# Performance work log

Hardware: AMD Instinct MI355X
Metric: run time of the kernel (lower is better)

The kernel has to match this reference:

```python
import math
import jax, jax.numpy as jnp
from jax import lax
import numpy as np

B, M, L = 256, 21, 512
P, S, D = 16, 8, 256
NL, EXP, H, LAM = 3, 2, 96, 0.01
T = (L - P) // S + 1  # 63 patches
HID = D * EXP


def _pos_enc():
    pe = np.zeros((T, D), np.float32)
    pos = np.arange(T, dtype=np.float32)[:, None]
    div = np.exp(np.arange(0, D, 2, dtype=np.float32) * (-math.log(10000.0) / D))
    pe[:, 0::2] = np.sin(pos * div)
    pe[:, 1::2] = np.cos(pos * div)
    return jnp.asarray(pe)


def _clin(zr, zi, Wr, Wi, br, bi):
    # faithful to torch: bias br added to both terms of yr (cancels), bi added twice in yi
    yr = (zr @ Wr.T + br) - (zi @ Wi.T + br)
    yi = (zr @ Wi.T + bi) + (zi @ Wr.T + bi)
    return yr, yi


def _softshrink(zr, zi):
    mag = jnp.sqrt(zr * zr + zi * zi)
    scale = jnp.maximum(mag - LAM, 0.0) / (mag + 1e-8) * (mag > LAM).astype(zr.dtype)
    return zr * scale, zi * scale


def _layernorm(x, g, b):
    mu = jnp.mean(x, -1, keepdims=True)
    var = jnp.mean((x - mu) ** 2, -1, keepdims=True)
    return (x - mu) / jnp.sqrt(var + 1e-5) * g + b


def _block(x, p):
    (Tw, Tb, Gew, Geb, Gpw, Gpb,
     H1Wr, H1Wi, H1br, H1bi, H2Wr, H2Wi, H2br, H2bi, lng, lnb) = p
    g = jax.nn.gelu(x @ Gew.T + Geb, approximate=False) @ Gpw.T + Gpb
    zf = jnp.fft.rfft(x, axis=1)  # FFT along time/patch axis T
    zr, zi = zf.real, zf.imag
    zr, zi = _clin(zr, zi, H1Wr, H1Wi, H1br, H1bi)
    zr, zi = _softshrink(zr, zi)
    zr, zi = _clin(zr, zi, H2Wr, H2Wi, H2br, H2bi)
    pt = jnp.fft.irfft(lax.complex(zr, zi), n=x.shape[1], axis=1)
    out = (g * pt) @ Tw.T + Tb
    return _layernorm(out + x, lng, lnb)


def _forward(x, conv_w, conv_b, tp, sp, gate_w, gate_b, proj_w, proj_b):
    # per-instance, per-variable norm over time (biased std, eps on std)
    mean = jnp.mean(x, -1, keepdims=True)
    std = jnp.sqrt(jnp.mean((x - mean) ** 2, -1, keepdims=True))
    xn = (x - mean) / (std + 1e-5)
    patches = lax.conv_general_dilated(xn, conv_w, (S,), 'VALID',
                                       dimension_numbers=('NCH', 'OIH', 'NCH'))
    patches = patches + conv_b[None, :, None]
    h = patches.transpose(0, 2, 1) + _pos_enc()[None]  # (B, T, D)
    t = h
    s = h
    for i in range(NL):
        t = _block(t, tuple(a[i] for a in tp))
        s = _block(s, tuple(a[i] for a in sp))
    gate = jax.nn.sigmoid(t @ gate_w.T + gate_b)
    feat = gate * t + (1.0 - gate) * s
    out = feat.reshape(feat.shape[0], -1) @ proj_w.T + proj_b
    y = out.reshape(-1, M, H) * (std + 1e-5) + mean
    return y


def setup_inputs() -> dict:
    key = jax.random.key(0)
    ks = iter(jax.random.split(key, 64))

    def nrm(shape, scale):
        return jax.random.normal(next(ks), shape, jnp.float32) * scale

    inp = {'x': nrm((B, M, L), 1.0)}
    inp['conv_w'] = nrm((D, M, P), 1.0 / math.sqrt(M * P))
    inp['conv_b'] = jnp.zeros((D,), jnp.float32)

    def layer_params(prefix):
        d = {}
        d[prefix + 'Tw'] = nrm((NL, D, D), 1.0 / math.sqrt(D))
        d[prefix + 'Tb'] = jnp.zeros((NL, D), jnp.float32)
        d[prefix + 'Gew'] = nrm((NL, HID, D), 1.0 / math.sqrt(D))
        d[prefix + 'Geb'] = jnp.zeros((NL, HID), jnp.float32)
        d[prefix + 'Gpw'] = nrm((NL, D, HID), 1.0 / math.sqrt(HID))
        d[prefix + 'Gpb'] = jnp.zeros((NL, D), jnp.float32)
        for hname in ('H1', 'H2'):
            d[prefix + hname + 'Wr'] = nrm((NL, D, D), 1.0 / math.sqrt(D))
            d[prefix + hname + 'Wi'] = nrm((NL, D, D), 1.0 / math.sqrt(D))
            d[prefix + hname + 'br'] = jnp.zeros((NL, D), jnp.float32)
            d[prefix + hname + 'bi'] = jnp.zeros((NL, D), jnp.float32)
        d[prefix + 'lng'] = jnp.ones((NL, D), jnp.float32)
        d[prefix + 'lnb'] = jnp.zeros((NL, D), jnp.float32)
        return d

    inp.update(layer_params('t_'))
    inp.update(layer_params('s_'))
    inp['gate_w'] = nrm((1, D), 1.0 / math.sqrt(D))
    inp['gate_b'] = jnp.zeros((1,), jnp.float32)
    inp['proj_w'] = nrm((M * H, T * D), 1.0 / math.sqrt(T * D))
    inp['proj_b'] = jnp.zeros((M * H,), jnp.float32)
    return inp


def reference(x, conv_w, conv_b,
              t_Tw, t_Tb, t_Gew, t_Geb, t_Gpw, t_Gpb,
              t_H1Wr, t_H1Wi, t_H1br, t_H1bi, t_H2Wr, t_H2Wi, t_H2br, t_H2bi, t_lng, t_lnb,
              s_Tw, s_Tb, s_Gew, s_Geb, s_Gpw, s_Gpb,
              s_H1Wr, s_H1Wi, s_H1br, s_H1bi, s_H2Wr, s_H2Wi, s_H2br, s_H2bi, s_lng, s_lnb,
              gate_w, gate_b, proj_w, proj_b):
    tp = (t_Tw, t_Tb, t_Gew, t_Geb, t_Gpw, t_Gpb,
          t_H1Wr, t_H1Wi, t_H1br, t_H1bi, t_H2Wr, t_H2Wi, t_H2br, t_H2bi, t_lng, t_lnb)
    sp = (s_Tw, s_Tb, s_Gew, s_Geb, s_Gpw, s_Gpb,
          s_H1Wr, s_H1Wi, s_H1br, s_H1bi, s_H2Wr, s_H2Wi, s_H2br, s_H2bi, s_lng, s_lnb)
    return _forward(x, conv_w, conv_b, tp, sp, gate_w, gate_b, proj_w, proj_b)
```

## Files before the change

kernel.cpp:

```cpp
#include <hip/hip_runtime.h>
#include <cstddef>
#include <cstdint>

#define B_    256
#define M_    21
#define L_    512
#define D_    256
#define T_    63
#define F_    32
#define NT_   16128
#define HID_  512
#define KCP_  352
#define H_    96
#define LAM_  0.01f
#define PZ_   16

typedef __attribute__((ext_vector_type(8))) short short8;
typedef __attribute__((ext_vector_type(4))) float f32x4;
typedef unsigned int u32;
typedef const u32 __attribute__((address_space(1)))* gas1_t;
typedef u32 __attribute__((address_space(3)))* las3_t;

__device__ __forceinline__ void async_copy16(const void* g, void* l) {
  __builtin_amdgcn_global_load_lds((gas1_t)g, (las3_t)(uintptr_t)l, 16, 0, 0);
}
__device__ __forceinline__ unsigned short f2bf(float x) {
  unsigned u = __float_as_uint(x);
  return (unsigned short)((u + 0x7FFF + ((u >> 16) & 1)) >> 16);
}
__device__ __forceinline__ float bf2f(unsigned short u) {
  return __uint_as_float(((unsigned)u) << 16);
}
__device__ __forceinline__ float gelu_exact(float v) {
  return 0.5f * v * (1.0f + erff(v * 0.70710678118654752f));
}
__device__ __forceinline__ float block_sum256(float v, float* red4) {
  #pragma unroll
  for (int off = 32; off > 0; off >>= 1) v += __shfl_down(v, off, 64);
  if ((threadIdx.x & 63) == 0) red4[threadIdx.x >> 6] = v;
  __syncthreads();
  float r = red4[0] + red4[1] + red4[2] + red4[3];
  __syncthreads();
  return r;
}
__device__ __forceinline__ float wave_sum(float v) {
  #pragma unroll
  for (int off = 1; off < 64; off <<= 1) v += __shfl_xor(v, off, 64);
  return v;
}

struct CvtEnt { const float* src; unsigned short* dst; int rows, scol, dcol, blk0; };
struct CvtArgs { CvtEnt e[19]; int nent; };
__global__ __launch_bounds__(256) void wprep_kernel(CvtArgs a) {
  int blk = blockIdx.x, e = 0;
  while (e + 1 < a.nent && a.e[e + 1].blk0 <= blk) ++e;
  CvtEnt en = a.e[e];
  int idx = (blk - en.blk0) * 256 + threadIdx.x;
  int total = en.rows * en.dcol;
  if (idx >= total) return;
  int r = idx / en.dcol, c = idx - r * en.dcol;
  float v = (c < en.scol) ? en.src[(size_t)r * en.scol + c] : 0.f;
  en.dst[idx] = f2bf(v);
}

struct CatArgs { const float* wr[12]; const float* wi[12]; };
__global__ __launch_bounds__(256) void wcat_kernel(CatArgs a, unsigned short* dst) {
  int e = blockIdx.x >> 10;
  int idx = ((blockIdx.x & 1023) << 8) + threadIdx.x;
  int r = idx >> 9, c = idx & 511;
  int cp = r >> 1, p = r & 1, d = c >> 1, q = c & 1;
  const float* wr = a.wr[e];
  const float* wi = a.wi[e];
  float v;
  if (p == 0) v = (q == 0) ? wr[cp * 256 + d] : -wi[cp * 256 + d];
  else        v = (q == 0) ? wi[cp * 256 + d] :  wr[cp * 256 + d];
  dst[(size_t)e * 262144 + idx] = f2bf(v);
}

template <int ACT, int OUTBF, int BIASM, int KSTEPS, int CVTA, int CVTW,
          int SHRINK, int MULPT, int SPLITK, int BK, int RT, int PEW>
__global__ __launch_bounds__(256) void mm_kernel(
    const void* __restrict__ Av,
    const unsigned short* __restrict__ W0, const unsigned short* __restrict__ W1,
    const float* __restrict__ Wf,
    const float* __restrict__ b0, const float* __restrict__ b1,
    const unsigned short* __restrict__ ptb,
    void* __restrict__ Cv,
    const int K, const int Dout, const int ksteps_rt, const int yhalf,
    const int prow, const int totk) {
  constexpr int NP = BK / 32;
  constexpr int RWS = 32 * RT;
  __shared__ __align__(16) unsigned short As[NP * RWS * 32];
  __shared__ __align__(16) unsigned short Bs[NP * 128 * 32];
  const int tid = threadIdx.x, w = tid >> 6, lane = tid & 63;
  const int quad = lane >> 4, r16 = lane & 15;
  int nks = KSTEPS ? KSTEPS : ksteps_rt;
  const int ksbeg = SPLITK ? (int)blockIdx.z * nks : 0;
  if (SPLITK) { int rem = totk - ksbeg; if (nks > rem) nks = rem; }
  const int kst = ksbeg * BK;
  const int tower = ((int)blockIdx.y >= yhalf) ? 1 : 0;
  const unsigned short* Wb = tower ? W1 : W0;
  const float* bias = tower ? b1 : b0;

  const unsigned short* Ab = (const unsigned short*)Av;
  const float* Af = (const float*)Av;
  const unsigned short* gA = nullptr;
  unsigned short* lA = As + (w * 8 * RT) * 32;
  if (!CVTA) gA = Ab + (size_t)((int)blockIdx.y * RWS + w * 8 * RT + (lane >> 2)) * K
                     + kst + (lane & 3) * 8;
  const unsigned short* gB = nullptr;
  unsigned short* lB = Bs + (w * 32) * 32;
  if (!CVTW) gB = Wb + (size_t)((int)blockIdx.x * 128 + w * 32 + (lane >> 2)) * K
                     + kst + (lane & 3) * 8;
  const int crow = tid >> 3;
  const int ck4  = (tid & 7) << 2;

  float4 areg[NP][RT];
  float4 wreg[NP][4];
  auto loadA = [&](int ksi) {
    #pragma unroll
    for (int p = 0; p < NP; ++p)
      #pragma unroll
      for (int rr = 0; rr < RT; ++rr)
        areg[p][rr] = *reinterpret_cast<const float4*>(
            Af + (size_t)((int)blockIdx.y * RWS + crow + 32 * rr) * K
               + kst + ksi * BK + p * 32 + ck4);
  };
  auto loadW = [&](int ksi) {
    #pragma unroll
    for (int p = 0; p < NP; ++p)
      #pragma unroll
      for (int rr = 0; rr < 4; ++rr) {
        int wrow = (int)blockIdx.x * 128 + crow + 32 * rr;
        if (wrow >= Dout) wrow = Dout - 1;
        wreg[p][rr] = *reinterpret_cast<const float4*>(
            Wf + (size_t)wrow * K + kst + ksi * BK + p * 32 + ck4);
      }
  };
  if (CVTA) loadA(0);
  if (CVTW) loadW(0);

  f32x4 acc[RT][4];
  #pragma unroll
  for (int i = 0; i < RT; ++i)
    #pragma unroll
    for (int j = 0; j < 4; ++j)
      #pragma unroll
      for (int r = 0; r < 4; ++r) acc[i][j][r] = 0.f;

  for (int ks = 0; ks < nks; ++ks) {
    if (!CVTA) {
      #pragma unroll
      for (int p = 0; p < NP; ++p)
        #pragma unroll
        for (int c = 0; c < RT / 2; ++c)
          async_copy16(gA + (size_t)(c * 16) * K + p * 32,
                       lA + p * (RWS * 32) + c * 16 * 32);
      gA += BK;
    } else {
      #pragma unroll
      for (int p = 0; p < NP; ++p)
        #pragma unroll
        for (int rr = 0; rr < RT; ++rr) {
          float4 v = areg[p][rr];
          ushort4 o; o.x = f2bf(v.x); o.y = f2bf(v.y); o.z = f2bf(v.z); o.w = f2bf(v.w);
          *reinterpret_cast<ushort4*>(As + p * (RWS * 32) + (crow + 32 * rr) * 32 + ck4) = o;
        }
    }
    if (!CVTW) {
      #pragma unroll
      for (int p = 0; p < NP; ++p) {
        async_copy16(gB + p * 32, lB + p * 4096);
        async_copy16(gB + (size_t)16 * K + p * 32, lB + p * 4096 + 16 * 32);
      }
      gB += BK;
    } else {
      #pragma unroll
      for (int p = 0; p < NP; ++p)
        #pragma unroll
        for (int rr = 0; rr < 4; ++rr) {
          float4 v = wreg[p][rr];
          ushort4 o; o.x = f2bf(v.x); o.y = f2bf(v.y); o.z = f2bf(v.z); o.w = f2bf(v.w);
          *reinterpret_cast<ushort4*>(Bs + p * 4096 + (crow + 32 * rr) * 32 + ck4) = o;
        }
    }
    __syncthreads();
    if (CVTA && ks + 1 < nks) loadA(ks + 1);
    if (CVTW && ks + 1 < nks) loadW(ks + 1);
    #pragma unroll
    for (int p = 0; p < NP; ++p) {
      const unsigned short* pa = As + p * (RWS * 32) + ((w >> 1) * 16 * RT + r16) * 32 + quad * 8;
      const unsigned short* pb = Bs + p * 4096 + (64 * (w & 1) + r16) * 32 + quad * 8;
      short8 af[RT], bfv[4];
      #pragma unroll
      for (int i = 0; i < RT; ++i) af[i] = *reinterpret_cast<const short8*>(pa + i * 512);
      #pragma unroll
      for (int j = 0; j < 4; ++j) bfv[j] = *reinterpret_cast<const short8*>(pb + j * 512);
      #pragma unroll
      for (int i = 0; i < RT; ++i)
        #pragma unroll
        for (int j = 0; j < 4; ++j)
          acc[i][j] = __builtin_amdgcn_mfma_f32_16x16x32_bf16(af[i], bfv[j], acc[i][j], 0, 0, 0);
    }
    __syncthreads();
  }

  float* Cf = (float*)Cv;
  unsigned short* Cb = (unsigned short*)Cv;
  if (SPLITK) Cf += (size_t)blockIdx.z * prow * Dout;
  const int colb = (int)blockIdx.x * 128 + 64 * (w & 1) + r16;
  const int rowb = (int)blockIdx.y * RWS + 16 * RT * (w >> 1) + quad * 4;
  #pragma unroll
  for (int j = 0; j < 4; ++j) {
    int col = colb + 16 * j;
    float bv = 0.f;
    if (BIASM == 0) bv = bias[col];
    else if (BIASM == 1) bv = (col & 1) ? 2.0f * bias[col >> 1] : 0.f;
    bool colok = (BIASM != 2) || (col < Dout);
    #pragma unroll
    for (int i = 0; i < RT; ++i) {
      #pragma unroll
      for (int r = 0; r < 4; ++r) {
        int row = rowb + 16 * i + r;
        float v = acc[i][j][r] + bv;
        if (ACT == 1) v = gelu_exact(v);
        if (SHRINK) {
          float o = __shfl_xor(v, 1, 64);
          float mag = sqrtf(v * v + o * o);
          float s = (mag > LAM_) ? (mag - LAM_) / (mag + 1e-8f) : 0.f;
          v *= s;
        }
        if (MULPT) v *= bf2f(ptb[(size_t)row * Dout + col]);
        if (colok) {
          if (PEW) {
            int t = row % T_;
            float freq = expf((float)(col & ~1) * (-9.210340371976184f / 256.0f));
            float ang = (float)t * freq;
            float pe = (col & 1) ? cosf(ang) : sinf(ang);
            float h = v + pe;
            Cf[(size_t)row * Dout + col] = h;
            Cf[(size_t)row * Dout + col + (size_t)NT_ * D_] = h;
          } else if (OUTBF) {
            Cb[(size_t)row * Dout + col] = f2bf(v);
          } else {
            Cf[(size_t)row * Dout + col] = v;
          }
        }
      }
    }
  }
}

__global__ __launch_bounds__(256) void twln_kernel(
    const unsigned short* __restrict__ A,
    const unsigned short* __restrict__ W0, const unsigned short* __restrict__ W1,
    const float* __restrict__ b0, const float* __restrict__ b1,
    const float* __restrict__ lg0, const float* __restrict__ lb0,
    const float* __restrict__ lg1, const float* __restrict__ lb1,
    float* __restrict__ x32) {
  __shared__ __align__(16) unsigned short As[2][64 * 32];
  __shared__ __align__(16) unsigned short Bs[2][256 * 32];
  const int tid = threadIdx.x, w = tid >> 6, lane = tid & 63;
  const int quad = lane >> 4, r16 = lane & 15;
  const int rh = w >> 1, ch = w & 1;
  const int by = blockIdx.x;
  const int tower = (by >= 252) ? 1 : 0;
  const unsigned short* W = tower ? W1 : W0;
  const float* bias = tower ? b1 : b0;
  const float* lng = tower ? lg1 : lg0;
  const float* lnb = tower ? lb1 : lb0;

  const unsigned short* gA = A + (size_t)(by * 64 + (tid >> 2)) * 256 + (tid & 3) * 8;
  const unsigned short* gW = W + (size_t)(tid >> 2) * 256 + (tid & 3) * 8;

  f32x4 acc[2][8];
  #pragma unroll
  for (int i = 0; i < 2; ++i)
    #pragma unroll
    for (int j = 0; j < 8; ++j)
      #pragma unroll
      for (int r = 0; r < 4; ++r) acc[i][j][r] = 0.f;

  for (int ks = 0; ks < 4; ++ks) {
    #pragma unroll
    for (int p = 0; p < 2; ++p)
      async_copy16(gA + p * 32, (char*)As + p * 4096 + tid * 16);
    #pragma unroll
    for (int p = 0; p < 2; ++p)
      #pragma unroll
      for (int k = 0; k < 4; ++k)
        async_copy16(gW + (size_t)k * 16384 + p * 32,
                     (char*)Bs + p * 16384 + k * 4096 + tid * 16);
    gA += 64; gW += 64;
    __syncthreads();
    #pragma unroll
    for (int p = 0; p < 2; ++p) {
      const unsigned short* pa = As[p] + (rh * 32 + r16) * 32 + quad * 8;
      const unsigned short* pb = Bs[p] + (ch * 128 + r16) * 32 + quad * 8;
      short8 af[2], bfv[8];
      #pragma unroll
      for (int i = 0; i < 2; ++i) af[i] = *reinterpret_cast<const short8*>(pa + i * 512);
      #pragma unroll
      for (int j = 0; j < 8; ++j) bfv[j] = *reinterpret_cast<const short8*>(pb + j * 512);
      #pragma unroll
      for (int i = 0; i < 2; ++i)
        #pragma unroll
        for (int j = 0; j < 8; ++j)
          acc[i][j] = __builtin_amdgcn_mfma_f32_16x16x32_bf16(af[i], bfv[j], acc[i][j], 0, 0, 0);
    }
    __syncthreads();
  }

  const int rowb = by * 64 + rh * 32 + quad * 4;
  const int colb = ch * 128 + r16;
  float s[2][4], sq[2][4];
  #pragma unroll
  for (int i = 0; i < 2; ++i)
    #pragma unroll
    for (int r = 0; r < 4; ++r) { s[i][r] = 0.f; sq[i][r] = 0.f; }
  #pragma unroll
  for (int j = 0; j < 8; ++j) {
    int col = colb + j * 16;
    float bv = bias[col];
    #pragma unroll
    for (int i = 0; i < 2; ++i)
      #pragma unroll
      for (int r = 0; r < 4; ++r) {
        int row = rowb + i * 16 + r;
        float h = acc[i][j][r] + bv + x32[(size_t)row * 256 + col];
        acc[i][j][r] = h;
        s[i][r] += h;
        sq[i][r] += h * h;
      }
  }
  #pragma unroll
  for (int off = 1; off < 16; off <<= 1)
    #pragma unroll
    for (int i = 0; i < 2; ++i)
      #pragma unroll
      for (int r = 0; r < 4; ++r) {
        s[i][r]  += __shfl_xor(s[i][r],  off, 64);
        sq[i][r] += __shfl_xor(sq[i][r], off, 64);
      }
  float* red = (float*)As;
  if (r16 == 0) {
    #pragma unroll
    for (int i = 0; i < 2; ++i)
      #pragma unroll
      for (int r = 0; r < 4; ++r) {
        int lr = rh * 32 + i * 16 + quad * 4 + r;
        red[lr * 4 + ch * 2]     = s[i][r];
        red[lr * 4 + ch * 2 + 1] = sq[i][r];
      }
  }
  __syncthreads();
  #pragma unroll
  for (int i = 0; i < 2; ++i)
    #pragma unroll
    for (int r = 0; r < 4; ++r) {
      int lr = rh * 32 + i * 16 + quad * 4 + r;
      float tot = red[lr * 4] + red[lr * 4 + 2];
      float tsq = red[lr * 4 + 1] + red[lr * 4 + 3];
      float mu = tot * (1.0f / 256.0f);
      float var = tsq * (1.0f / 256.0f) - mu * mu;
      float is = rsqrtf(var + 1e-5f);
      int row = rowb + i * 16 + r;
      #pragma unroll
      for (int j = 0; j < 8; ++j) {
        int col = colb + j * 16;
        x32[(size_t)row * 256 + col] = (acc[i][j][r] - mu) * is * lng[col] + lnb[col];
      }
    }
}

__global__ __launch_bounds__(256) void norm_kernel(const float* __restrict__ x,
    float* __restrict__ xn, float* __restrict__ meanb, float* __restrict__ stdb) {
  __shared__ float red[4];
  int bm = blockIdx.x;
  const float* xr = x + (size_t)bm * L_;
  float v0 = xr[threadIdx.x], v1 = xr[threadIdx.x + 256];
  float mu = block_sum256(v0 + v1, red) * (1.0f / L_);
  float d0 = v0 - mu, d1 = v1 - mu;
  float sd = sqrtf(block_sum256(d0 * d0 + d1 * d1, red) * (1.0f / L_));
  float inv = 1.0f / (sd + 1e-5f);
  float* xo = xn + (size_t)bm * L_;
  xo[threadIdx.x] = d0 * inv;
  xo[threadIdx.x + 256] = d1 * inv;
  if (threadIdx.x == 0) { meanb[bm] = mu; stdb[bm] = sd; }
}

__global__ __launch_bounds__(256) void im2col_kernel(const float* __restrict__ xn,
                                                     unsigned short* __restrict__ im) {
  int row = blockIdx.x;
  int b = row / T_, t = row - b * T_;
  const float* xb = xn + (size_t)b * M_ * L_ + t * 8;
  unsigned short* o = im + (size_t)row * KCP_;
  for (int i = threadIdx.x; i < KCP_; i += 256) {
    float v = 0.f;
    if (i < 336) { int m = i >> 4, p = i & 15; v = xb[m * L_ + p]; }
    o[i] = f2bf(v);
  }
}

__global__ __launch_bounds__(256) void dft_kernel(const float* __restrict__ X,
                                                  unsigned short* __restrict__ Zcat) {
  __shared__ float2 tw[T_ * F_];
  int bt = blockIdx.x, d = threadIdx.x;
  for (int i = threadIdx.x; i < T_ * F_; i += 256) {
    int t = i >> 5, f = i & 31;
    int k = (f * t) % T_;
    float sn, cs;
    sincosf((6.283185307179586f / 63.0f) * (float)k, &sn, &cs);
    tw[i] = make_float2(cs, -sn);
  }
  __syncthreads();
  const float* xb = X + (size_t)bt * T_ * D_ + d;
  float ar[F_], ai[F_];
  #pragma unroll
  for (int f = 0; f < F_; ++f) { ar[f] = 0.f; ai[f] = 0.f; }
  for (int t = 0; t < T_; ++t) {
    float v = xb[(size_t)t * D_];
    const float2* w = &tw[t * F_];
    #pragma unroll
    for (int f = 0; f < F_; ++f) {
      float2 c = w[f];
      ar[f] = fmaf(v, c.x, ar[f]);
      ai[f] = fmaf(v, c.y, ai[f]);
    }
  }
  u32* z = reinterpret_cast<u32*>(Zcat + (size_t)bt * F_ * 512);
  #pragma unroll
  for (int f = 0; f < F_; ++f)
    z[f * 256 + d] = (u32)f2bf(ar[f]) | ((u32)f2bf(ai[f]) << 16);
}

__global__ __launch_bounds__(256) void irfft_kernel(const unsigned short* __restrict__ Y,
                                                    unsigned short* __restrict__ ptb) {
  __shared__ float2 tw[T_ * 31];
  int bt = blockIdx.x, d = threadIdx.x;
  for (int i = threadIdx.x; i < T_ * 31; i += 256) {
    int t = i / 31, f = i - t * 31 + 1;
    int k = (f * t) % T_;
    float sn, cs;
    sincosf((6.283185307179586f / 63.0f) * (float)k, &sn, &cs);
    tw[i] = make_float2(cs * (2.0f / 63.0f), -sn * (2.0f / 63.0f));
  }
  __syncthreads();
  const unsigned short* yb = Y + (size_t)bt * F_ * 512 + 2 * d;
  float y0 = bf2f(yb[0]) * (1.0f / 63.0f);
  float yr[31], yi[31];
  #pragma unroll
  for (int f = 1; f < F_; ++f) {
    u32 p = *reinterpret_cast<const u32*>(yb + (size_t)f * 512);
    yr[f - 1] = bf2f((unsigned short)(p & 0xffff));
    yi[f - 1] = bf2f((unsigned short)(p >> 16));
  }
  unsigned short* po = ptb + (size_t)bt * T_ * D_ + d;
  for (int t = 0; t < T_; ++t) {
    const float2* w = &tw[t * 31];
    float acc0 = y0, acc1 = 0.f;
    #pragma unroll
    for (int f = 0; f < 31; f += 2) {
      float2 c = w[f];
      acc0 = fmaf(yr[f], c.x, fmaf(yi[f], c.y, acc0));
      if (f + 1 < 31) {
        float2 c1 = w[f + 1];
        acc1 = fmaf(yr[f + 1], c1.x, fmaf(yi[f + 1], c1.y, acc1));
      }
    }
    po[(size_t)t * D_] = f2bf(acc0 + acc1);
  }
}

__global__ __launch_bounds__(256) void gate_feat_kernel(const float* __restrict__ x32,
    const float* __restrict__ gw, const float* __restrict__ gb,
    unsigned short* __restrict__ featbf) {
  int row = blockIdx.x * 4 + (threadIdx.x >> 6);
  int lane = threadIdx.x & 63;
  size_t base = (size_t)row * D_ + lane * 4;
  float4 tv = *reinterpret_cast<const float4*>(x32 + base);
  float4 sv = *reinterpret_cast<const float4*>(x32 + base + (size_t)NT_ * D_);
  float4 gv = *reinterpret_cast<const float4*>(gw + lane * 4);
  float dot = wave_sum(tv.x * gv.x + tv.y * gv.y + tv.z * gv.z + tv.w * gv.w) + gb[0];
  float gate = 1.0f / (1.0f + expf(-dot));
  ushort4 o;
  o.x = f2bf(gate * tv.x + (1.0f - gate) * sv.x);
  o.y = f2bf(gate * tv.y + (1.0f - gate) * sv.y);
  o.z = f2bf(gate * tv.z + (1.0f - gate) * sv.z);
  o.w = f2bf(gate * tv.w + (1.0f - gate) * sv.w);
  *reinterpret_cast<ushort4*>(featbf + base) = o;
}

__global__ __launch_bounds__(256) void final_kernel(const float* __restrict__ part,
    const float* __restrict__ pb, const float* __restrict__ stdb,
    const float* __restrict__ meanb, float* __restrict__ y) {
  int i = blockIdx.x * 256 + threadIdx.x;
  float acc = 0.f;
  #pragma unroll
  for (int z = 0; z < PZ_; ++z) acc += part[(size_t)z * 516096 + i];
  int b = i / 2016;
  int col = i - b * 2016;
  int m = col / H_;
  float sc = stdb[b * M_ + m] + 1e-5f;
  y[i] = (acc + pb[col]) * sc + meanb[b * M_ + m];
}

extern "C" void kernel_launch(void* const* d_in, const int* in_sizes, int n_in,
                              void* d_out, int out_size, void* d_ws, size_t ws_size,
                              hipStream_t stream) {
  const float* x      = (const float*)d_in[0];
  const float* conv_w = (const float*)d_in[1];
  const float* conv_b = (const float*)d_in[2];
  const float* tP[16];
  const float* sP[16];
  for (int i = 0; i < 16; ++i) tP[i] = (const float*)d_in[3 + i];
  for (int i = 0; i < 16; ++i) sP[i] = (const float*)d_in[19 + i];
  const float* gate_w = (const float*)d_in[35];
  const float* gate_b = (const float*)d_in[36];
  const float* proj_w = (const float*)d_in[37];
  const float* proj_b = (const float*)d_in[38];
  float* out = (float*)d_out;

  float* ws    = (float*)d_ws;
  float* x32   = ws;
  unsigned short* wb = (unsigned short*)(x32 + 8257536);
  float* meanb = x32 + 8257536 + 2600960;
  float* stdb  = meanb + 5376;
  float* R1    = stdb + 5376 + 16;
  float* R2    = R1 + 8388608;

  unsigned short* im2colB = (unsigned short*)R1;
  unsigned short* Zcat    = (unsigned short*)R1;
  unsigned short* Ycat1   = (unsigned short*)(R1 + 4194304);
  unsigned short* ptb     = (unsigned short*)(R1 + 4194304);
  unsigned short* gp      = (unsigned short*)R1;
  unsigned short* featbf  = (unsigned short*)R1;

  float* xn     = R2;
  unsigned short* Ycat2b = (unsigned short*)R2;
  unsigned short* hidB = (unsigned short*)R2;
  float* part   = R2;

  unsigned short* convW = wb;
  unsigned short* sets  = wb + 90112;
  unsigned short* catW  = wb + 90112 + 1966080;

  CvtArgs ca; int blk0 = 0, ne = 0;
  auto add_ent = [&](const float* s, unsigned short* d, int rows, int scol, int dcol) {
    ca.e[ne].src = s; ca.e[ne].dst = d; ca.e[ne].rows = rows;
    ca.e[ne].scol = scol; ca.e[ne].dcol = dcol; ca.e[ne].blk0 = blk0;
    blk0 += (rows * dcol + 255) / 256; ++ne;
  };
  add_ent(conv_w, convW, 256, 336, 352);
  for (int tw = 0; tw < 2; ++tw) {
    const float** Pp = tw ? (const float**)sP : (const float**)tP;
    for (int l = 0; l < 3; ++l) {
      unsigned short* sb = sets + (size_t)(tw * 3 + l) * 327680;
      add_ent(Pp[2] + (size_t)l * 131072, sb,          512, 256, 256);
      add_ent(Pp[4] + (size_t)l * 131072, sb + 131072, 256, 512, 512);
      add_ent(Pp[0] + (size_t)l * 65536,  sb + 262144, 256, 256, 256);
    }
  }
  ca.nent = ne;
  wprep_kernel<<<blk0, 256, 0, stream>>>(ca);

  CatArgs cat;
  for (int tw = 0; tw < 2; ++tw) {
    const float** Pp = tw ? (const float**)sP : (const float**)tP;
    for (int l = 0; l < 3; ++l) {
      int e0 = (tw * 3 + l) * 2;
      cat.wr[e0]     = Pp[6]  + (size_t)l * 65536;
      cat.wi[e0]     = Pp[7]  + (size_t)l * 65536;
      cat.wr[e0 + 1] = Pp[10] + (size_t)l * 65536;
      cat.wi[e0 + 1] = Pp[11] + (size_t)l * 65536;
    }
  }
  wcat_kernel<<<12 * 1024, 256, 0, stream>>>(cat, catW);

  norm_kernel<<<B_ * M_, 256, 0, stream>>>(x, xn, meanb, stdb);
  im2col_kernel<<<NT_, 256, 0, stream>>>(xn, im2colB);
  mm_kernel<0, 0, 0, 11, 0, 0, 0, 0, 0, 32, 2, 1><<<dim3(2, 252), 256, 0, stream>>>(
      im2colB, convW, convW, nullptr, conv_b, conv_b, nullptr, x32,
      KCP_, 256, 0, 1 << 30, 0, 0);

  for (int l = 0; l < 3; ++l) {
    unsigned short* st0 = sets + (size_t)l * 327680;
    unsigned short* st1 = sets + (size_t)(3 + l) * 327680;
    unsigned short* c1t0 = catW + (size_t)((0 + l) * 2) * 262144;
    unsigned short* c2t0 = c1t0 + 262144;
    unsigned short* c1t1 = catW + (size_t)((3 + l) * 2) * 262144;
    unsigned short* c2t1 = c1t1 + 262144;

    dft_kernel<<<2 * B_, 256, 0, stream>>>(x32, Zcat);
    mm_kernel<0, 1, 1, 8, 0, 0, 1, 0, 0, 64, 2, 0><<<dim3(4, 256), 256, 0, stream>>>(
        Zcat, c1t0, c1t1, nullptr, tP[9] + (size_t)l * D_, sP[9] + (size_t)l * D_,
        nullptr, Ycat1, 512, 512, 0, 128, 0, 0);
    mm_kernel<0, 1, 1, 8, 0, 0, 0, 0, 0, 64, 2, 0><<<dim3(4, 256), 256, 0, stream>>>(
        Ycat1, c2t0, c2t1, nullptr, tP[13] + (size_t)l * D_, sP[13] + (size_t)l * D_,
        nullptr, Ycat2b, 512, 512, 0, 128, 0, 0);
    irfft_kernel<<<2 * B_, 256, 0, stream>>>(Ycat2b, ptb);
    mm_kernel<1, 1, 0, 4, 1, 0, 0, 0, 0, 64, 2, 0><<<dim3(4, 504), 256, 0, stream>>>(
        x32, st0, st1, nullptr, tP[3] + (size_t)l * HID_, sP[3] + (size_t)l * HID_,
        nullptr, hidB, 256, 512, 0, 252, 0, 0);
    mm_kernel<0, 1, 0, 8, 0, 0, 0, 1, 0, 64, 2, 0><<<dim3(2, 504), 256, 0, stream>>>(
        hidB, st0 + 131072, st1 + 131072, nullptr,
        tP[5] + (size_t)l * D_, sP[5] + (size_t)l * D_, ptb, gp, 512, 256, 0, 252, 0, 0);
    twln_kernel<<<504, 256, 0, stream>>>(
        gp, st0 + 262144, st1 + 262144,
        tP[1] + (size_t)l * D_, sP[1] + (size_t)l * D_,
        tP[14] + (size_t)l * D_, tP[15] + (size_t)l * D_,
        sP[14] + (size_t)l * D_, sP[15] + (size_t)l * D_, x32);
  }

  gate_feat_kernel<<<NT_ / 4, 256, 0, stream>>>(x32, gate_w, gate_b, featbf);
  mm_kernel<0, 0, 2, 0, 0, 1, 0, 0, 1, 64, 2, 0><<<dim3(16, 4, PZ_), 256, 0, stream>>>(
      featbf, nullptr, nullptr, proj_w, nullptr, nullptr, nullptr, part,
      NT_, 2016, 16, 1 << 30, 256, 252);
  final_kernel<<<2016, 256, 0, stream>>>(part, proj_b, stdb, meanb, out);
}
```

Measured before the change: 984.0 us.

## Fuse im2col into norm kernel and share layer-0 input across both towers

The normalization kernel now writes bf16 im2col patches directly, which removes the separate fp32 normalized buffer and the im2col kernel. Both towers start from the same embedding, so the conv epilogue writes it once. In layer 0 the tower-1 blocks of the DFT, H1 and gate matmuls and the residual read in twln are redirected to the tower-0 copy through a negative offset, and the DFT runs only half its blocks. This saves duplicated writes, reads and one launch, at the cost of scattered 2-byte stores in the norm kernel and extra offset logic.

```diff
diff --git a/kernel.cpp b/kernel.cpp
--- a/kernel.cpp
+++ b/kernel.cpp
@@ -87,7 +87,7 @@
     const unsigned short* __restrict__ ptb,
     void* __restrict__ Cv,
     const int K, const int Dout, const int ksteps_rt, const int yhalf,
-    const int prow, const int totk) {
+    const int prow, const int totk, const int asub) {
   constexpr int NP = BK / 32;
   constexpr int RWS = 32 * RT;
   __shared__ __align__(16) unsigned short As[NP * RWS * 32];
@@ -99,6 +99,7 @@
   if (SPLITK) { int rem = totk - ksbeg; if (nks > rem) nks = rem; }
   const int kst = ksbeg * BK;
   const int tower = ((int)blockIdx.y >= yhalf) ? 1 : 0;
+  const long long ao = tower ? (long long)asub : 0;
   const unsigned short* Wb = tower ? W1 : W0;
   const float* bias = tower ? b1 : b0;
 
@@ -106,8 +107,8 @@
   const float* Af = (const float*)Av;
   const unsigned short* gA = nullptr;
   unsigned short* lA = As + (w * 8 * RT) * 32;
-  if (!CVTA) gA = Ab + (size_t)((int)blockIdx.y * RWS + w * 8 * RT + (lane >> 2)) * K
-                     + kst + (lane & 3) * 8;
+  if (!CVTA) gA = Ab + ((size_t)((int)blockIdx.y * RWS + w * 8 * RT + (lane >> 2)) * K
+                     + kst + (lane & 3) * 8) - ao;
   const unsigned short* gB = nullptr;
   unsigned short* lB = Bs + (w * 32) * 32;
   if (!CVTW) gB = Wb + (size_t)((int)blockIdx.x * 128 + w * 32 + (lane >> 2)) * K
@@ -123,8 +124,8 @@
       #pragma unroll
       for (int rr = 0; rr < RT; ++rr)
         areg[p][rr] = *reinterpret_cast<const float4*>(
-            Af + (size_t)((int)blockIdx.y * RWS + crow + 32 * rr) * K
-               + kst + ksi * BK + p * 32 + ck4);
+            Af + ((size_t)((int)blockIdx.y * RWS + crow + 32 * rr) * K
+               + kst + ksi * BK + p * 32 + ck4) - ao);
   };
   auto loadW = [&](int ksi) {
     #pragma unroll
@@ -237,9 +238,7 @@
             float freq = expf((float)(col & ~1) * (-9.210340371976184f / 256.0f));
             float ang = (float)t * freq;
             float pe = (col & 1) ? cosf(ang) : sinf(ang);
-            float h = v + pe;
-            Cf[(size_t)row * Dout + col] = h;
-            Cf[(size_t)row * Dout + col + (size_t)NT_ * D_] = h;
+            Cf[(size_t)row * Dout + col] = v + pe;
           } else if (OUTBF) {
             Cb[(size_t)row * Dout + col] = f2bf(v);
           } else {
@@ -257,7 +256,7 @@
     const float* __restrict__ b0, const float* __restrict__ b1,
     const float* __restrict__ lg0, const float* __restrict__ lb0,
     const float* __restrict__ lg1, const float* __restrict__ lb1,
-    float* __restrict__ x32) {
+    float* __restrict__ x32, const int ressub) {
   __shared__ __align__(16) unsigned short As[2][64 * 32];
   __shared__ __align__(16) unsigned short Bs[2][256 * 32];
   const int tid = threadIdx.x, w = tid >> 6, lane = tid & 63;
@@ -265,6 +264,7 @@
   const int rh = w >> 1, ch = w & 1;
   const int by = blockIdx.x;
   const int tower = (by >= 252) ? 1 : 0;
+  const long long ro = tower ? (long long)ressub : 0;
   const unsigned short* W = tower ? W1 : W0;
   const float* bias = tower ? b1 : b0;
   const float* lng = tower ? lg1 : lg0;
@@ -327,7 +327,7 @@
       #pragma unroll
       for (int r = 0; r < 4; ++r) {
         int row = rowb + i * 16 + r;
-        float h = acc[i][j][r] + bv + x32[(size_t)row * 256 + col];
+        float h = acc[i][j][r] + bv + x32[((size_t)row * 256 + col) - ro];
         acc[i][j][r] = h;
         s[i][r] += h;
         sq[i][r] += h * h;
@@ -374,32 +374,33 @@
 }
 
 __global__ __launch_bounds__(256) void norm_kernel(const float* __restrict__ x,
-    float* __restrict__ xn, float* __restrict__ meanb, float* __restrict__ stdb) {
+    unsigned short* __restrict__ im, float* __restrict__ meanb, float* __restrict__ stdb) {
   __shared__ float red[4];
   int bm = blockIdx.x;
+  int b = bm / M_, m = bm - b * M_;
   const float* xr = x + (size_t)bm * L_;
   float v0 = xr[threadIdx.x], v1 = xr[threadIdx.x + 256];
   float mu = block_sum256(v0 + v1, red) * (1.0f / L_);
   float d0 = v0 - mu, d1 = v1 - mu;
   float sd = sqrtf(block_sum256(d0 * d0 + d1 * d1, red) * (1.0f / L_));
   float inv = 1.0f / (sd + 1e-5f);
-  float* xo = xn + (size_t)bm * L_;
-  xo[threadIdx.x] = d0 * inv;
-  xo[threadIdx.x + 256] = d1 * inv;
+  unsigned short* imb = im + (size_t)b * T_ * KCP_ + m * 16;
+  auto scat = [&](int l, float v) {
+    unsigned short o = f2bf(v);
+    int t0 = l >> 3, p0 = l & 7;
+    if (t0 < T_) imb[(size_t)t0 * KCP_ + p0] = o;
+    if (t0 >= 1) imb[(size_t)(t0 - 1) * KCP_ + p0 + 8] = o;
+  };
+  scat(threadIdx.x, d0 * inv);
+  scat(threadIdx.x + 256, d1 * inv);
+  if (m == 0) {
+    unsigned short* pz = im + (size_t)b * T_ * KCP_ + 336;
+    for (int i = threadIdx.x; i < T_ * 16; i += 256) {
+      int t = i >> 4, c = i & 15;
+      pz[(size_t)t * KCP_ + c] = 0;
+    }
+  }
   if (threadIdx.x == 0) { meanb[bm] = mu; stdb[bm] = sd; }
-}
-
-__global__ __launch_bounds__(256) void im2col_kernel(const float* __restrict__ xn,
-                                                     unsigned short* __restrict__ im) {
-  int row = blockIdx.x;
-  int b = row / T_, t = row - b * T_;
-  const float* xb = xn + (size_t)b * M_ * L_ + t * 8;
-  unsigned short* o = im + (size_t)row * KCP_;
-  for (int i = threadIdx.x; i < KCP_; i += 256) {
-    float v = 0.f;
-    if (i < 336) { int m = i >> 4, p = i & 15; v = xb[m * L_ + p]; }
-    o[i] = f2bf(v);
-  }
 }
 
 __global__ __launch_bounds__(256) void dft_kernel(const float* __restrict__ X,
@@ -536,7 +537,6 @@
   unsigned short* gp      = (unsigned short*)R1;
   unsigned short* featbf  = (unsigned short*)R1;
 
-  float* xn     = R2;
   unsigned short* Ycat2b = (unsigned short*)R2;
   unsigned short* hidB = (unsigned short*)R2;
   float* part   = R2;
@@ -577,11 +577,10 @@
   }
   wcat_kernel<<<12 * 1024, 256, 0, stream>>>(cat, catW);
 
-  norm_kernel<<<B_ * M_, 256, 0, stream>>>(x, xn, meanb, stdb);
-  im2col_kernel<<<NT_, 256, 0, stream>>>(xn, im2colB);
+  norm_kernel<<<B_ * M_, 256, 0, stream>>>(x, im2colB, meanb, stdb);
   mm_kernel<0, 0, 0, 11, 0, 0, 0, 0, 0, 32, 2, 1><<<dim3(2, 252), 256, 0, stream>>>(
       im2colB, convW, convW, nullptr, conv_b, conv_b, nullptr, x32,
-      KCP_, 256, 0, 1 << 30, 0, 0);
+      KCP_, 256, 0, 1 << 30, 0, 0, 0);
 
   for (int l = 0; l < 3; ++l) {
     unsigned short* st0 = sets + (size_t)l * 327680;
@@ -590,31 +589,34 @@
     unsigned short* c2t0 = c1t0 + 262144;
     unsigned short* c1t1 = catW + (size_t)((3 + l) * 2) * 262144;
     unsigned short* c2t1 = c1t1 + 262144;
-
-    dft_kernel<<<2 * B_, 256, 0, stream>>>(x32, Zcat);
+    const int aH1 = (l == 0) ? 8192 * 512 : 0;
+    const int aGe = (l == 0) ? NT_ * D_ : 0;
+
+    dft_kernel<<<(l == 0 ? B_ : 2 * B_), 256, 0, stream>>>(x32, Zcat);
     mm_kernel<0, 1, 1, 8, 0, 0, 1, 0, 0, 64, 2, 0><<<dim3(4, 256), 256, 0, stream>>>(
         Zcat, c1t0, c1t1, nullptr, tP[9] + (size_t)l * D_, sP[9] + (size_t)l * D_,
-        nullptr, Ycat1, 512, 512, 0, 128, 0, 0);
+        nullptr, Ycat1, 512, 512, 0, 128, 0, 0, aH1);
     mm_kernel<0, 1, 1, 8, 0, 0, 0, 0, 0, 64, 2, 0><<<dim3(4, 256), 256, 0, stream>>>(
         Ycat1, c2t0, c2t1, nullptr, tP[13] + (size_t)l * D_, sP[13] + (size_t)l * D_,
-        nullptr, Ycat2b, 512, 512, 0, 128, 0, 0);
+        nullptr, Ycat2b, 512, 512, 0, 128, 0, 0, 0);
     irfft_kernel<<<2 * B_, 256, 0, stream>>>(Ycat2b, ptb);
     mm_kernel<1, 1, 0, 4, 1, 0, 0, 0, 0, 64, 2, 0><<<dim3(4, 504), 256, 0, stream>>>(
         x32, st0, st1, nullptr, tP[3] + (size_t)l * HID_, sP[3] + (size_t)l * HID_,
-        nullptr, hidB, 256, 512, 0, 252, 0, 0);
+        nullptr, hidB, 256, 512, 0, 252, 0, 0, aGe);
     mm_kernel<0, 1, 0, 8, 0, 0, 0, 1, 0, 64, 2, 0><<<dim3(2, 504), 256, 0, stream>>>(
         hidB, st0 + 131072, st1 + 131072, nullptr,
-        tP[5] + (size_t)l * D_, sP[5] + (size_t)l * D_, ptb, gp, 512, 256, 0, 252, 0, 0);
+        tP[5] + (size_t)l * D_, sP[5] + (size_t)l * D_, ptb, gp, 512, 256, 0, 252, 0, 0, 0);
     twln_kernel<<<504, 256, 0, stream>>>(
         gp, st0 + 262144, st1 + 262144,
         tP[1] + (size_t)l * D_, sP[1] + (size_t)l * D_,
         tP[14] + (size_t)l * D_, tP[15] + (size_t)l * D_,
-        sP[14] + (size_t)l * D_, sP[15] + (size_t)l * D_, x32);
+        sP[14] + (size_t)l * D_, sP[15] + (size_t)l * D_, x32,
+        (l == 0) ? NT_ * D_ : 0);
   }
 
   gate_feat_kernel<<<NT_ / 4, 256, 0, stream>>>(x32, gate_w, gate_b, featbf);
   mm_kernel<0, 0, 2, 0, 0, 1, 0, 0, 1, 64, 2, 0><<<dim3(16, 4, PZ_), 256, 0, stream>>>(
       featbf, nullptr, nullptr, proj_w, nullptr, nullptr, nullptr, part,
-      NT_, 2016, 16, 1 << 30, 256, 252);
+      NT_, 2016, 16, 1 << 30, 256, 252, 0);
   final_kernel<<<2016, 256, 0, stream>>>(part, proj_b, stdb, meanb, out);
 }
```

After: 957.9 us. 2.7% less time.
